# Kernel tuning notes

Hardware: AMD Instinct MI355X
Metric: run time of the kernel (lower is better)

Reference implementation:

```python
import jax, jax.numpy as jnp
import numpy as np

N_NODES = 50000
N_EDGES = 800000
IN_CH = 128
OUT_CH = 64
HEADS = 4
NEG_SLOPE = 0.2  # PyG GATConv default


def setup_inputs() -> dict:
    key = jax.random.key(0)
    k1, k2, k3, k4, k5 = jax.random.split(key, 5)
    x = jax.random.normal(k1, (N_NODES, IN_CH), dtype=jnp.float32)
    edge_index = jax.random.randint(k2, (2, N_EDGES), 0, N_NODES, dtype=jnp.int64)
    W = jax.random.normal(k3, (HEADS * OUT_CH, IN_CH), dtype=jnp.float32) * (1.0 / np.sqrt(IN_CH))
    att_src = jax.random.normal(k4, (HEADS, OUT_CH), dtype=jnp.float32) * (1.0 / np.sqrt(OUT_CH))
    att_dst = jax.random.normal(k5, (HEADS, OUT_CH), dtype=jnp.float32) * (1.0 / np.sqrt(OUT_CH))
    bias = jnp.zeros((OUT_CH,), dtype=jnp.float32)
    return {"x": x, "edge_index": edge_index, "W": W,
            "att_src": att_src, "att_dst": att_dst, "bias": bias}


def reference(x, edge_index, W, att_src, att_dst, bias):
    # GAT2NO_NORM.forward in eval mode: dropout == identity.
    N = x.shape[0]
    H, C = att_src.shape
    # PyG GATConv adds self-loops by default.
    loop = jnp.arange(N, dtype=edge_index.dtype)
    src = jnp.concatenate([edge_index[0], loop])  # message source j
    dst = jnp.concatenate([edge_index[1], loop])  # message target i
    # Linear projection, reshape to heads: [N, H, C]
    h = (x @ W.T).reshape(N, H, C)
    # Per-node attention halves: [N, H]
    a_src = jnp.einsum('nhc,hc->nh', h, att_src)
    a_dst = jnp.einsum('nhc,hc->nh', h, att_dst)
    # Per-edge raw score, LeakyReLU: [E, H]
    e = jax.nn.leaky_relu(a_src[src] + a_dst[dst], NEG_SLOPE)
    # Segment (edge-)softmax over incoming edges of each dst node.
    m = jax.lax.stop_gradient(jax.ops.segment_max(e, dst, num_segments=N))
    ex = jnp.exp(e - m[dst])
    denom = jax.ops.segment_sum(ex, dst, num_segments=N)
    alpha = ex / denom[dst]  # self-loops guarantee denom > 0
    # Weighted scatter-sum of messages: [N, H, C]
    msg = h[src] * alpha[:, :, None]
    out = jax.ops.segment_sum(msg, dst, num_segments=N)
    # concat=False -> mean over heads, then bias, then ReLU (module wrapper)
    out = out.mean(axis=1) + bias
    return jax.nn.relu(out)
```

## Files before the change

kernel.cpp:

```cpp
#include <hip/hip_runtime.h>
#include <hip/hip_fp16.h>
#include <math.h>

#define N_NODES 50000
#define N_EDGES 800000
#define IN_CH 128
#define PROJ_CH 256
#define OUT_CH 64
#define HEADS 4
#define NEG_SLOPE 0.2f
#define CAP 80

typedef _Float16 f16x8 __attribute__((ext_vector_type(8)));
typedef _Float16 f16x4 __attribute__((ext_vector_type(4)));
typedef float    f32x4 __attribute__((ext_vector_type(4)));

__device__ __forceinline__ float leaky(float v) {
    return v > 0.f ? v : NEG_SLOPE * v;
}

__global__ __launch_bounds__(256) void init_cnt_kernel(int* __restrict__ cnt) {
    int i = blockIdx.x * 256 + threadIdx.x;
    if (i < N_NODES) cnt[i] = 0;
}

__global__ __launch_bounds__(256) void wfrag_prep_kernel(
    const float* __restrict__ W, _Float16* __restrict__ Wfrag)
{
    int t = blockIdx.x * 256 + threadIdx.x;
    if (t >= 4096) return;
    int lane = t & 63;
    int n0i  = (t >> 6) & 3;
    int w    = (t >> 8) & 3;
    int k0i  = t >> 10;
    int oc = w * 64 + n0i * 16 + (lane & 15);
    int kb = k0i * 32 + (lane >> 4) * 8;
    const float* src = W + (size_t)oc * IN_CH + kb;
    f16x8 v;
#pragma unroll
    for (int j = 0; j < 8; ++j) v[j] = (_Float16)src[j];
    *(f16x8*)(Wfrag + (size_t)t * 8) = v;
}

__global__ __launch_bounds__(256) void proj_mfma_kernel(
    const float* __restrict__ x, const _Float16* __restrict__ Wfrag,
    const float* __restrict__ att_src, const float* __restrict__ att_dst,
    _Float16* __restrict__ h, float* __restrict__ a_src, float* __restrict__ a_dst)
{
    __shared__ _Float16 xs[64 * 136];
    const int tid  = threadIdx.x;
    const int w    = tid >> 6;
    const int lane = tid & 63;
    const int q    = lane >> 4;
    const int l15  = lane & 15;
    const int nb   = blockIdx.x * 64;

    f16x8 B[4][4];
#pragma unroll
    for (int k0i = 0; k0i < 4; ++k0i)
#pragma unroll
        for (int n0i = 0; n0i < 4; ++n0i)
            B[k0i][n0i] = *(const f16x8*)(Wfrag +
                (size_t)(((k0i * 4 + w) * 4 + n0i) * 64 + lane) * 8);

#pragma unroll
    for (int r = 0; r < 8; ++r) {
        int v   = r * 256 + tid;
        int row = v >> 5;
        int c4  = v & 31;
        int grow = nb + row;
        if (grow > N_NODES - 1) grow = N_NODES - 1;
        float4 xv = *(const float4*)(x + (size_t)grow * IN_CH + c4 * 4);
        f16x4 hv;
        hv[0] = (_Float16)xv.x; hv[1] = (_Float16)xv.y;
        hv[2] = (_Float16)xv.z; hv[3] = (_Float16)xv.w;
        *(f16x4*)&xs[row * 136 + c4 * 4] = hv;
    }
    __syncthreads();

    f32x4 acc[4][4];
#pragma unroll
    for (int m0i = 0; m0i < 4; ++m0i)
#pragma unroll
        for (int n0i = 0; n0i < 4; ++n0i)
            acc[m0i][n0i] = (f32x4){0.f, 0.f, 0.f, 0.f};

#pragma unroll
    for (int k0i = 0; k0i < 4; ++k0i) {
        f16x8 A[4];
#pragma unroll
        for (int m0i = 0; m0i < 4; ++m0i)
            A[m0i] = *(const f16x8*)&xs[(m0i * 16 + l15) * 136 + k0i * 32 + q * 8];
#pragma unroll
        for (int n0i = 0; n0i < 4; ++n0i)
#pragma unroll
            for (int m0i = 0; m0i < 4; ++m0i)
                acc[m0i][n0i] = __builtin_amdgcn_mfma_f32_16x16x32_f16(
                    A[m0i], B[k0i][n0i], acc[m0i][n0i], 0, 0, 0);
    }

    float att_s[4], att_d[4];
#pragma unroll
    for (int n0i = 0; n0i < 4; ++n0i) {
        att_s[n0i] = att_src[w * 64 + n0i * 16 + l15];
        att_d[n0i] = att_dst[w * 64 + n0i * 16 + l15];
    }

#pragma unroll
    for (int m0i = 0; m0i < 4; ++m0i) {
        float vs[4], vd[4];
#pragma unroll
        for (int r = 0; r < 4; ++r) {
            float s = 0.f, d = 0.f;
#pragma unroll
            for (int n0i = 0; n0i < 4; ++n0i) {
                s = fmaf(acc[m0i][n0i][r], att_s[n0i], s);
                d = fmaf(acc[m0i][n0i][r], att_d[n0i], d);
            }
            vs[r] = s; vd[r] = d;
        }
#pragma unroll
        for (int off = 1; off < 16; off <<= 1) {
#pragma unroll
            for (int r = 0; r < 4; ++r) {
                vs[r] += __shfl_xor(vs[r], off, 64);
                vd[r] += __shfl_xor(vd[r], off, 64);
            }
        }
#pragma unroll
        for (int r = 0; r < 4; ++r) {
            int node = nb + m0i * 16 + q * 4 + r;
            if (l15 == 0 && node < N_NODES) {
                a_src[node * HEADS + w] = vs[r];
                a_dst[node * HEADS + w] = vd[r];
            }
        }
#pragma unroll
        for (int r = 0; r < 4; ++r) {
            int node = nb + m0i * 16 + q * 4 + r;
            if (node < N_NODES) {
#pragma unroll
                for (int n0i = 0; n0i < 4; ++n0i)
                    h[(size_t)node * PROJ_CH + w * 64 + n0i * 16 + l15] =
                        (_Float16)acc[m0i][n0i][r];
            }
        }
    }
}

__global__ __launch_bounds__(256) void fill_bucket_kernel(
    const int* __restrict__ ei, int* __restrict__ cnt, int* __restrict__ csr)
{
    int e = blockIdx.x * 256 + threadIdx.x;
    if (e < N_EDGES) {
        int src = ei[e];
        int dst = ei[N_EDGES + e];
        int pos = atomicAdd(&cnt[dst], 1);
        if (pos < CAP) csr[dst * CAP + pos] = src;
    }
}

__global__ __launch_bounds__(256) void aggregate_kernel(
    const __half* __restrict__ h, const float* __restrict__ a_src,
    const float* __restrict__ a_dst, const int* __restrict__ cnt,
    const int* __restrict__ csr, const float* __restrict__ bias,
    float* __restrict__ out)
{
    const int tid  = threadIdx.x;
    const int wave = tid >> 6;
    const int l    = tid & 63;
    const int i    = blockIdx.x * 4 + wave;

    __shared__ float lw_all[4][(CAP + 1) * 4];
    __shared__ int   lj_all[4][CAP + 1 + 3];
    float* lw = lw_all[wave];
    int*   lj = lj_all[wave];

    const int n    = min(cnt[i], CAP);
    const int base = i * CAP;
    const int h4   = l & 3;
    const float adh = a_dst[i * 4 + h4];

    float lsum = 0.f;
    {
        float ws = __expf(leaky(a_src[i * 4 + h4] + adh));
        if (l < 4) { lw[l] = ws; lsum = ws; }
        if (l == 0) lj[0] = i;
    }

    const int erel = l >> 2;
    for (int p0 = 0; p0 < n; p0 += 16) {
        int e = p0 + erel;
        bool valid = e < n;
        int j = valid ? csr[base + e] : 0;
        float w = 0.f;
        if (valid) w = __expf(leaky(a_src[j * 4 + h4] + adh));
        lsum += w;
        lw[(e + 1) * 4 + h4] = w;
        if (h4 == 0) lj[e + 1] = j;
    }
#pragma unroll
    for (int off = 4; off < 64; off <<= 1) lsum += __shfl_xor(lsum, off, 64);

    __syncthreads();

    const int half_ = l >> 5;
    const int jj    = l & 31;
    const int hd    = jj >> 3;
    const int m_total = n + 1;
    const uint4* hv = (const uint4*)h;

    float acc[8];
#pragma unroll
    for (int k = 0; k < 8; ++k) acc[k] = 0.f;

    for (int q = 0; q < m_total; q += 2) {
        int e = q + half_;
        int idx = (e < m_total) ? e : 0;
        float w = (e < m_total) ? lw[idx * 4 + hd] : 0.f;
        int j = lj[idx];
        uint4 d = hv[(size_t)j * 32 + jj];
        float2 f0 = __half22float2(*(const __half2*)&d.x);
        float2 f1 = __half22float2(*(const __half2*)&d.y);
        float2 f2 = __half22float2(*(const __half2*)&d.z);
        float2 f3 = __half22float2(*(const __half2*)&d.w);
        acc[0] = fmaf(w, f0.x, acc[0]);
        acc[1] = fmaf(w, f0.y, acc[1]);
        acc[2] = fmaf(w, f1.x, acc[2]);
        acc[3] = fmaf(w, f1.y, acc[3]);
        acc[4] = fmaf(w, f2.x, acc[4]);
        acc[5] = fmaf(w, f2.y, acc[5]);
        acc[6] = fmaf(w, f3.x, acc[6]);
        acc[7] = fmaf(w, f3.y, acc[7]);
    }

#pragma unroll
    for (int k = 0; k < 8; ++k) acc[k] += __shfl_xor(acc[k], 32, 64);

    float linv = 1.f / __shfl(lsum, hd, 64);
#pragma unroll
    for (int k = 0; k < 8; ++k) {
        float r = acc[k] * linv;
        r += __shfl_xor(r, 8, 64);
        r += __shfl_xor(r, 16, 64);
        acc[k] = r;
    }

    if (l < 8) {
        float* op = out + (size_t)i * OUT_CH + l * 8;
        float4 o0, o1;
        o0.x = fmaxf(0.25f * acc[0] + bias[l * 8 + 0], 0.f);
        o0.y = fmaxf(0.25f * acc[1] + bias[l * 8 + 1], 0.f);
        o0.z = fmaxf(0.25f * acc[2] + bias[l * 8 + 2], 0.f);
        o0.w = fmaxf(0.25f * acc[3] + bias[l * 8 + 3], 0.f);
        o1.x = fmaxf(0.25f * acc[4] + bias[l * 8 + 4], 0.f);
        o1.y = fmaxf(0.25f * acc[5] + bias[l * 8 + 5], 0.f);
        o1.z = fmaxf(0.25f * acc[6] + bias[l * 8 + 6], 0.f);
        o1.w = fmaxf(0.25f * acc[7] + bias[l * 8 + 7], 0.f);
        *(float4*)op = o0;
        *((float4*)op + 1) = o1;
    }
}

extern "C" void kernel_launch(void* const* d_in, const int* in_sizes, int n_in,
                              void* d_out, int out_size, void* d_ws, size_t ws_size,
                              hipStream_t stream)
{
    const float* x       = (const float*)d_in[0];
    const int*   ei      = (const int*)d_in[1];
    const float* W       = (const float*)d_in[2];
    const float* att_src = (const float*)d_in[3];
    const float* att_dst = (const float*)d_in[4];
    const float* bias    = (const float*)d_in[5];
    float* out = (float*)d_out;

    _Float16* h   = (_Float16*)d_ws;
    _Float16* Wfrag = h + (size_t)N_NODES * PROJ_CH;
    float* asrc  = (float*)(Wfrag + 4096 * 8);
    float* adst  = asrc + (size_t)N_NODES * HEADS;
    int*   cnt   = (int*)(adst + (size_t)N_NODES * HEADS);
    int*   csr   = cnt + N_NODES;

    hipLaunchKernelGGL(init_cnt_kernel, dim3((N_NODES + 255) / 256), dim3(256), 0, stream,
                       cnt);
    hipLaunchKernelGGL(wfrag_prep_kernel, dim3(16), dim3(256), 0, stream,
                       W, Wfrag);
    hipLaunchKernelGGL(proj_mfma_kernel, dim3((N_NODES + 63) / 64), dim3(256), 0, stream,
                       x, Wfrag, att_src, att_dst, h, asrc, adst);
    hipLaunchKernelGGL(fill_bucket_kernel, dim3((N_EDGES + 255) / 256), dim3(256), 0, stream,
                       ei, cnt, (int*)csr);
    hipLaunchKernelGGL(aggregate_kernel, dim3(N_NODES / 4), dim3(256), 0, stream,
                       (const __half*)h, asrc, adst, cnt, csr, bias, out);
}
```

Measured before the change: 216.5 us.

## Fuse edge bucketing into projection kernel, use 16-bit CSR, unroll aggregation

Merges count-zeroing with weight-fragment prep, and folds the edge bucket fill into the MFMA projection kernel, going from five launches to three. The edge indices are loaded at the start of the projection kernel so their latency overlaps the GEMM work. CSR source indices are stored as unsigned short, which is valid because node ids stay below 65536, and this halves CSR traffic. The aggregation loop is unrolled to keep two gathers in flight per thread, at the cost of more registers and atomics now issued inside the projection kernel.

```diff
diff --git a/kernel.cpp b/kernel.cpp
--- a/kernel.cpp
+++ b/kernel.cpp
@@ -10,6 +10,8 @@
 #define HEADS 4
 #define NEG_SLOPE 0.2f
 #define CAP 80
+#define PROJ_BLOCKS 782
+#define EPB 1024
 
 typedef _Float16 f16x8 __attribute__((ext_vector_type(8)));
 typedef _Float16 f16x4 __attribute__((ext_vector_type(4)));
@@ -19,32 +21,30 @@
     return v > 0.f ? v : NEG_SLOPE * v;
 }
 
-__global__ __launch_bounds__(256) void init_cnt_kernel(int* __restrict__ cnt) {
-    int i = blockIdx.x * 256 + threadIdx.x;
-    if (i < N_NODES) cnt[i] = 0;
-}
-
-__global__ __launch_bounds__(256) void wfrag_prep_kernel(
-    const float* __restrict__ W, _Float16* __restrict__ Wfrag)
+__global__ __launch_bounds__(256) void prep_kernel(
+    const float* __restrict__ W, _Float16* __restrict__ Wfrag, int* __restrict__ cnt)
 {
     int t = blockIdx.x * 256 + threadIdx.x;
-    if (t >= 4096) return;
-    int lane = t & 63;
-    int n0i  = (t >> 6) & 3;
-    int w    = (t >> 8) & 3;
-    int k0i  = t >> 10;
-    int oc = w * 64 + n0i * 16 + (lane & 15);
-    int kb = k0i * 32 + (lane >> 4) * 8;
-    const float* src = W + (size_t)oc * IN_CH + kb;
-    f16x8 v;
-#pragma unroll
-    for (int j = 0; j < 8; ++j) v[j] = (_Float16)src[j];
-    *(f16x8*)(Wfrag + (size_t)t * 8) = v;
-}
-
-__global__ __launch_bounds__(256) void proj_mfma_kernel(
+    if (t < N_NODES) cnt[t] = 0;
+    if (t < 4096) {
+        int lane = t & 63;
+        int n0i  = (t >> 6) & 3;
+        int w    = (t >> 8) & 3;
+        int k0i  = t >> 10;
+        int oc = w * 64 + n0i * 16 + (lane & 15);
+        int kb = k0i * 32 + (lane >> 4) * 8;
+        const float* src = W + (size_t)oc * IN_CH + kb;
+        f16x8 v;
+#pragma unroll
+        for (int j = 0; j < 8; ++j) v[j] = (_Float16)src[j];
+        *(f16x8*)(Wfrag + (size_t)t * 8) = v;
+    }
+}
+
+__global__ __launch_bounds__(256) void proj_fill_kernel(
     const float* __restrict__ x, const _Float16* __restrict__ Wfrag,
     const float* __restrict__ att_src, const float* __restrict__ att_dst,
+    const int* __restrict__ ei, int* __restrict__ cnt, unsigned short* __restrict__ csr,
     _Float16* __restrict__ h, float* __restrict__ a_src, float* __restrict__ a_dst)
 {
     __shared__ _Float16 xs[64 * 136];
@@ -54,6 +54,15 @@
     const int q    = lane >> 4;
     const int l15  = lane & 15;
     const int nb   = blockIdx.x * 64;
+
+    int esrc[4], edst[4];
+    const int ebase = blockIdx.x * EPB + tid;
+#pragma unroll
+    for (int k = 0; k < 4; ++k) {
+        int e = ebase + k * 256;
+        if (e < N_EDGES) { esrc[k] = ei[e]; edst[k] = ei[N_EDGES + e]; }
+        else edst[k] = -1;
+    }
 
     f16x8 B[4][4];
 #pragma unroll
@@ -146,24 +155,20 @@
             }
         }
     }
-}
-
-__global__ __launch_bounds__(256) void fill_bucket_kernel(
-    const int* __restrict__ ei, int* __restrict__ cnt, int* __restrict__ csr)
-{
-    int e = blockIdx.x * 256 + threadIdx.x;
-    if (e < N_EDGES) {
-        int src = ei[e];
-        int dst = ei[N_EDGES + e];
-        int pos = atomicAdd(&cnt[dst], 1);
-        if (pos < CAP) csr[dst * CAP + pos] = src;
+
+#pragma unroll
+    for (int k = 0; k < 4; ++k) {
+        if (edst[k] >= 0) {
+            int pos = atomicAdd(&cnt[edst[k]], 1);
+            if (pos < CAP) csr[edst[k] * CAP + pos] = (unsigned short)esrc[k];
+        }
     }
 }
 
 __global__ __launch_bounds__(256) void aggregate_kernel(
-    const __half* __restrict__ h, const float* __restrict__ a_src,
+    const _Float16* __restrict__ h, const float* __restrict__ a_src,
     const float* __restrict__ a_dst, const int* __restrict__ cnt,
-    const int* __restrict__ csr, const float* __restrict__ bias,
+    const unsigned short* __restrict__ csr, const float* __restrict__ bias,
     float* __restrict__ out)
 {
     const int tid  = threadIdx.x;
@@ -192,7 +197,7 @@
     for (int p0 = 0; p0 < n; p0 += 16) {
         int e = p0 + erel;
         bool valid = e < n;
-        int j = valid ? csr[base + e] : 0;
+        int j = valid ? (int)csr[base + e] : 0;
         float w = 0.f;
         if (valid) w = __expf(leaky(a_src[j * 4 + h4] + adh));
         lsum += w;
@@ -214,24 +219,41 @@
 #pragma unroll
     for (int k = 0; k < 8; ++k) acc[k] = 0.f;
 
-    for (int q = 0; q < m_total; q += 2) {
-        int e = q + half_;
-        int idx = (e < m_total) ? e : 0;
-        float w = (e < m_total) ? lw[idx * 4 + hd] : 0.f;
-        int j = lj[idx];
-        uint4 d = hv[(size_t)j * 32 + jj];
-        float2 f0 = __half22float2(*(const __half2*)&d.x);
-        float2 f1 = __half22float2(*(const __half2*)&d.y);
-        float2 f2 = __half22float2(*(const __half2*)&d.z);
-        float2 f3 = __half22float2(*(const __half2*)&d.w);
-        acc[0] = fmaf(w, f0.x, acc[0]);
-        acc[1] = fmaf(w, f0.y, acc[1]);
-        acc[2] = fmaf(w, f1.x, acc[2]);
-        acc[3] = fmaf(w, f1.y, acc[3]);
-        acc[4] = fmaf(w, f2.x, acc[4]);
-        acc[5] = fmaf(w, f2.y, acc[5]);
-        acc[6] = fmaf(w, f3.x, acc[6]);
-        acc[7] = fmaf(w, f3.y, acc[7]);
+    for (int qq = 0; qq < m_total; qq += 4) {
+        int e0 = qq + half_;
+        int e1 = e0 + 2;
+        int i0 = (e0 < m_total) ? e0 : 0;
+        int i1 = (e1 < m_total) ? e1 : 0;
+        float w0 = (e0 < m_total) ? lw[i0 * 4 + hd] : 0.f;
+        float w1 = (e1 < m_total) ? lw[i1 * 4 + hd] : 0.f;
+        int j0 = lj[i0];
+        int j1 = lj[i1];
+        uint4 d0 = hv[(size_t)j0 * 32 + jj];
+        uint4 d1 = hv[(size_t)j1 * 32 + jj];
+        float2 a0 = __half22float2(*(const __half2*)&d0.x);
+        float2 a1 = __half22float2(*(const __half2*)&d0.y);
+        float2 a2 = __half22float2(*(const __half2*)&d0.z);
+        float2 a3 = __half22float2(*(const __half2*)&d0.w);
+        acc[0] = fmaf(w0, a0.x, acc[0]);
+        acc[1] = fmaf(w0, a0.y, acc[1]);
+        acc[2] = fmaf(w0, a1.x, acc[2]);
+        acc[3] = fmaf(w0, a1.y, acc[3]);
+        acc[4] = fmaf(w0, a2.x, acc[4]);
+        acc[5] = fmaf(w0, a2.y, acc[5]);
+        acc[6] = fmaf(w0, a3.x, acc[6]);
+        acc[7] = fmaf(w0, a3.y, acc[7]);
+        float2 b0 = __half22float2(*(const __half2*)&d1.x);
+        float2 b1 = __half22float2(*(const __half2*)&d1.y);
+        float2 b2 = __half22float2(*(const __half2*)&d1.z);
+        float2 b3 = __half22float2(*(const __half2*)&d1.w);
+        acc[0] = fmaf(w1, b0.x, acc[0]);
+        acc[1] = fmaf(w1, b0.y, acc[1]);
+        acc[2] = fmaf(w1, b1.x, acc[2]);
+        acc[3] = fmaf(w1, b1.y, acc[3]);
+        acc[4] = fmaf(w1, b2.x, acc[4]);
+        acc[5] = fmaf(w1, b2.y, acc[5]);
+        acc[6] = fmaf(w1, b3.x, acc[6]);
+        acc[7] = fmaf(w1, b3.y, acc[7]);
     }
 
 #pragma unroll
@@ -274,21 +296,17 @@
     const float* bias    = (const float*)d_in[5];
     float* out = (float*)d_out;
 
-    _Float16* h   = (_Float16*)d_ws;
+    _Float16* h     = (_Float16*)d_ws;
     _Float16* Wfrag = h + (size_t)N_NODES * PROJ_CH;
     float* asrc  = (float*)(Wfrag + 4096 * 8);
     float* adst  = asrc + (size_t)N_NODES * HEADS;
     int*   cnt   = (int*)(adst + (size_t)N_NODES * HEADS);
-    int*   csr   = cnt + N_NODES;
-
-    hipLaunchKernelGGL(init_cnt_kernel, dim3((N_NODES + 255) / 256), dim3(256), 0, stream,
-                       cnt);
-    hipLaunchKernelGGL(wfrag_prep_kernel, dim3(16), dim3(256), 0, stream,
-                       W, Wfrag);
-    hipLaunchKernelGGL(proj_mfma_kernel, dim3((N_NODES + 63) / 64), dim3(256), 0, stream,
-                       x, Wfrag, att_src, att_dst, h, asrc, adst);
-    hipLaunchKernelGGL(fill_bucket_kernel, dim3((N_EDGES + 255) / 256), dim3(256), 0, stream,
-                       ei, cnt, (int*)csr);
+    unsigned short* csr = (unsigned short*)(cnt + N_NODES);
+
+    hipLaunchKernelGGL(prep_kernel, dim3(196), dim3(256), 0, stream,
+                       W, Wfrag, cnt);
+    hipLaunchKernelGGL(proj_fill_kernel, dim3(PROJ_BLOCKS), dim3(256), 0, stream,
+                       x, Wfrag, att_src, att_dst, ei, cnt, csr, h, asrc, adst);
     hipLaunchKernelGGL(aggregate_kernel, dim3(N_NODES / 4), dim3(256), 0, stream,
-                       (const __half*)h, asrc, adst, cnt, csr, bias, out);
-}
+                       h, asrc, adst, cnt, csr, bias, out);
+}
```

Measured after the change: 206.3 us. 4.7% less time.
